# Optimization experiments

Hardware: AMD Instinct MI355X
Metric: run time of the kernel (lower is better)

## Reference

```python
import jax, jax.numpy as jnp
import numpy as np


def setup_inputs() -> dict:
    key = jax.random.key(0)
    k1, k2 = jax.random.split(key)
    B, S, H = 8, 4096, 1024
    sequence_output = jax.random.normal(k1, (B, S, H), dtype=jnp.float32)
    # labels in {0,1}: no -100 padding so the mask-compaction has a static shape
    sent_token_mask = jax.random.randint(k2, (B, S), 0, 2, dtype=jnp.int64)
    return {"sequence_output": sequence_output, "sent_token_mask": sent_token_mask}


def reference(sequence_output, sent_token_mask):
    B, S, H = sequence_output.shape
    # mask compaction: all positions valid (labels in {0,1}), so it's a reshape
    sent_features = sequence_output.reshape(B * S, H)  # [B*S, H]

    labels = sent_token_mask  # [B, S]
    # seg_id assigned BEFORE processing each label; increments AFTER label==0
    inc = (labels == 0).astype(jnp.int32).reshape(B * S)
    within = jnp.cumsum(inc) - inc  # exclusive prefix sum of increments
    # extra increment at end of each example whose last label == 1
    extra = (labels[:, -1] == 1).astype(jnp.int32)  # [B]
    extra_off = jnp.cumsum(extra) - extra           # exclusive over examples
    topic_segment_ids = within.reshape(B, S) + extra_off[:, None]
    return sent_features, topic_segment_ids.reshape(B * S)
```

## Files before the change

kernel.cpp:

```cpp
#include <hip/hip_runtime.h>

constexpr int Bn  = 8;
constexpr int Sn  = 4096;
constexpr int Nn  = Bn * Sn;
constexpr int Hn  = 1024;

constexpr int TPB = 256;
constexpr int NW  = TPB / 64;
constexpr int G4    = Nn / 4;
constexpr int ITERS = G4 / TPB;

constexpr size_t FEAT_ELEMS = (size_t)Nn * Hn;
constexpr size_t FEAT_VEC4  = FEAT_ELEMS / 4;
constexpr int    VEC_PER_T  = 8;
constexpr int    COPY_BLOCKS = (int)(FEAT_VEC4 / ((size_t)TPB * VEC_PER_T));

typedef float v4f __attribute__((ext_vector_type(4)));

__global__ __launch_bounds__(TPB) void fused_kernel(const float* __restrict__ seq,
                                                    const int* __restrict__ labels,
                                                    float* __restrict__ out) {
    if (blockIdx.x > 0) {
        const v4f* __restrict__ src = reinterpret_cast<const v4f*>(seq);
        v4f* __restrict__ dst       = reinterpret_cast<v4f*>(out);
        const size_t base = (size_t)(blockIdx.x - 1) * (TPB * VEC_PER_T) + threadIdx.x;
        v4f r[VEC_PER_T];
#pragma unroll
        for (int i = 0; i < VEC_PER_T; ++i)
            r[i] = __builtin_nontemporal_load(&src[base + (size_t)i * TPB]);
#pragma unroll
        for (int i = 0; i < VEC_PER_T; ++i)
            __builtin_nontemporal_store(r[i], &dst[base + (size_t)i * TPB]);
        return;
    }

    __shared__ int range_pre[TPB];
    __shared__ int wave_sums[NW];
    __shared__ int extra_off_sh[Bn];

    const int tid  = threadIdx.x;
    const int lane = tid & 63;
    const int hl   = lane & 31;
    const int wave = tid >> 6;

    const int4* __restrict__ lab4 = reinterpret_cast<const int4*>(labels);
    v4f* __restrict__ seg4 = reinterpret_cast<v4f*>(out + FEAT_ELEMS);

#pragma unroll 4
    for (int i = 0; i < ITERS; ++i) {
        const int g = i * TPB + tid;
        int4 v = lab4[g];
        int c = (v.x == 0) + (v.y == 0) + (v.z == 0) + (v.w == 0);
#pragma unroll
        for (int k = 1; k < 32; k <<= 1) c += __shfl_xor(c, k, 32);
        if (hl == 0) range_pre[g >> 5] = c;
    }

    if (tid == 0) {
        int acc = 0;
#pragma unroll
        for (int b = 0; b < Bn; ++b) {
            extra_off_sh[b] = acc;
            acc += (labels[b * Sn + Sn - 1] == 1);
        }
    }
    __syncthreads();

    const int s = range_pre[tid];
    int incl = s;
#pragma unroll
    for (int off = 1; off < 64; off <<= 1) {
        int u = __shfl_up(incl, off, 64);
        if (lane >= off) incl += u;
    }
    if (lane == 63) wave_sums[wave] = incl;
    __syncthreads();

    if (wave == 0) {
        int v = (lane < NW) ? wave_sums[lane] : 0;
#pragma unroll
        for (int off = 1; off < NW; off <<= 1) {
            int u = __shfl_up(v, off, 64);
            if (lane >= off) v += u;
        }
        if (lane < NW) wave_sums[lane] = v;
    }
    __syncthreads();

    range_pre[tid] = (wave ? wave_sums[wave - 1] : 0) + (incl - s);
    __syncthreads();

#pragma unroll 4
    for (int i = 0; i < ITERS; ++i) {
        const int g = i * TPB + tid;
        int4 v = lab4[g];
        const int f0 = (v.x == 0), f1 = (v.y == 0), f2 = (v.z == 0), f3 = (v.w == 0);
        const int c = f0 + f1 + f2 + f3;
        int pc = c;
#pragma unroll
        for (int off = 1; off < 32; off <<= 1) {
            int u = __shfl_up(pc, off, 32);
            if (hl >= off) pc += u;
        }
        const int base = range_pre[g >> 5] + extra_off_sh[g >> 10] + (pc - c);
        v4f r;
        r.x = (float)base;
        r.y = (float)(base + f0);
        r.z = (float)(base + f0 + f1);
        r.w = (float)(base + f0 + f1 + f2);
        __builtin_nontemporal_store(r, &seg4[g]);
    }
}

extern "C" void kernel_launch(void* const* d_in, const int* in_sizes, int n_in,
                              void* d_out, int out_size, void* d_ws, size_t ws_size,
                              hipStream_t stream) {
    const float* seq    = (const float*)d_in[0];
    const int*   labels = (const int*)d_in[1];
    float*       out    = (float*)d_out;

    fused_kernel<<<COPY_BLOCKS + 1, TPB, 0, stream>>>(seq, labels, out);
}
```

Baseline: 233.4 us.

## Split feature copy into hipMemcpyAsync and single-pass tiled segment scan

Replaces the fused kernel's copy blocks with a device-to-device hipMemcpyAsync for the 128 MiB feature tensor. The segment-id computation becomes its own one-block, 1024-thread kernel that does a single-pass tiled scan with a running carry and prefetching, instead of reading the labels twice. The aim is to use the runtime's optimized copy path and shorten the scan. In exchange the copy and the scan now run one after another rather than concurrently, and there are two launches instead of one.

After: 234.1 us. Within noise of the previous version (+0.3%).

```diff
diff --git a/kernel.cpp b/kernel.cpp
--- a/kernel.cpp
+++ b/kernel.cpp
@@ -5,110 +5,77 @@
 constexpr int Nn  = Bn * Sn;
 constexpr int Hn  = 1024;
 
-constexpr int TPB = 256;
-constexpr int NW  = TPB / 64;
+constexpr size_t FEAT_ELEMS = (size_t)Nn * Hn;
+constexpr size_t FEAT_BYTES = FEAT_ELEMS * sizeof(float);
+
+constexpr int STPB  = 1024;
+constexpr int SNW   = STPB / 64;
 constexpr int G4    = Nn / 4;
-constexpr int ITERS = G4 / TPB;
-
-constexpr size_t FEAT_ELEMS = (size_t)Nn * Hn;
-constexpr size_t FEAT_VEC4  = FEAT_ELEMS / 4;
-constexpr int    VEC_PER_T  = 8;
-constexpr int    COPY_BLOCKS = (int)(FEAT_VEC4 / ((size_t)TPB * VEC_PER_T));
+constexpr int TILES = G4 / STPB;
 
 typedef float v4f __attribute__((ext_vector_type(4)));
 
-__global__ __launch_bounds__(TPB) void fused_kernel(const float* __restrict__ seq,
-                                                    const int* __restrict__ labels,
-                                                    float* __restrict__ out) {
-    if (blockIdx.x > 0) {
-        const v4f* __restrict__ src = reinterpret_cast<const v4f*>(seq);
-        v4f* __restrict__ dst       = reinterpret_cast<v4f*>(out);
-        const size_t base = (size_t)(blockIdx.x - 1) * (TPB * VEC_PER_T) + threadIdx.x;
-        v4f r[VEC_PER_T];
-#pragma unroll
-        for (int i = 0; i < VEC_PER_T; ++i)
-            r[i] = __builtin_nontemporal_load(&src[base + (size_t)i * TPB]);
-#pragma unroll
-        for (int i = 0; i < VEC_PER_T; ++i)
-            __builtin_nontemporal_store(r[i], &dst[base + (size_t)i * TPB]);
-        return;
-    }
-
-    __shared__ int range_pre[TPB];
-    __shared__ int wave_sums[NW];
-    __shared__ int extra_off_sh[Bn];
+__global__ __launch_bounds__(STPB) void seg_kernel(const int* __restrict__ labels,
+                                                   float* __restrict__ out) {
+    __shared__ int wsums[SNW];
+    __shared__ int extra_sh[Bn];
 
     const int tid  = threadIdx.x;
     const int lane = tid & 63;
-    const int hl   = lane & 31;
     const int wave = tid >> 6;
 
     const int4* __restrict__ lab4 = reinterpret_cast<const int4*>(labels);
     v4f* __restrict__ seg4 = reinterpret_cast<v4f*>(out + FEAT_ELEMS);
 
-#pragma unroll 4
-    for (int i = 0; i < ITERS; ++i) {
-        const int g = i * TPB + tid;
-        int4 v = lab4[g];
-        int c = (v.x == 0) + (v.y == 0) + (v.z == 0) + (v.w == 0);
-#pragma unroll
-        for (int k = 1; k < 32; k <<= 1) c += __shfl_xor(c, k, 32);
-        if (hl == 0) range_pre[g >> 5] = c;
-    }
-
     if (tid == 0) {
         int acc = 0;
 #pragma unroll
         for (int b = 0; b < Bn; ++b) {
-            extra_off_sh[b] = acc;
+            extra_sh[b] = acc;
             acc += (labels[b * Sn + Sn - 1] == 1);
         }
     }
+
+    int carry = 0;
+    int4 v = lab4[tid];
     __syncthreads();
 
-    const int s = range_pre[tid];
-    int incl = s;
-#pragma unroll
-    for (int off = 1; off < 64; off <<= 1) {
-        int u = __shfl_up(incl, off, 64);
-        if (lane >= off) incl += u;
-    }
-    if (lane == 63) wave_sums[wave] = incl;
-    __syncthreads();
+    for (int k = 0; k < TILES; ++k) {
+        int4 nv;
+        if (k + 1 < TILES) nv = lab4[(k + 1) * STPB + tid];
 
-    if (wave == 0) {
-        int v = (lane < NW) ? wave_sums[lane] : 0;
-#pragma unroll
-        for (int off = 1; off < NW; off <<= 1) {
-            int u = __shfl_up(v, off, 64);
-            if (lane >= off) v += u;
-        }
-        if (lane < NW) wave_sums[lane] = v;
-    }
-    __syncthreads();
-
-    range_pre[tid] = (wave ? wave_sums[wave - 1] : 0) + (incl - s);
-    __syncthreads();
-
-#pragma unroll 4
-    for (int i = 0; i < ITERS; ++i) {
-        const int g = i * TPB + tid;
-        int4 v = lab4[g];
         const int f0 = (v.x == 0), f1 = (v.y == 0), f2 = (v.z == 0), f3 = (v.w == 0);
         const int c = f0 + f1 + f2 + f3;
-        int pc = c;
+
+        int incl = c;
 #pragma unroll
-        for (int off = 1; off < 32; off <<= 1) {
-            int u = __shfl_up(pc, off, 32);
-            if (hl >= off) pc += u;
+        for (int off = 1; off < 64; off <<= 1) {
+            int u = __shfl_up(incl, off, 64);
+            if (lane >= off) incl += u;
         }
-        const int base = range_pre[g >> 5] + extra_off_sh[g >> 10] + (pc - c);
+        if (lane == 63) wsums[wave] = incl;
+        __syncthreads();
+
+        int wexcl = 0, tot = 0;
+#pragma unroll
+        for (int w = 0; w < SNW; ++w) {
+            int s = wsums[w];
+            wexcl += (w < wave) ? s : 0;
+            tot   += s;
+        }
+
+        const int g    = k * STPB + tid;
+        const int base = carry + wexcl + (incl - c) + extra_sh[g >> 10];
         v4f r;
         r.x = (float)base;
         r.y = (float)(base + f0);
         r.z = (float)(base + f0 + f1);
         r.w = (float)(base + f0 + f1 + f2);
         __builtin_nontemporal_store(r, &seg4[g]);
+
+        carry += tot;
+        __syncthreads();
+        v = nv;
     }
 }
 
@@ -119,5 +86,7 @@
     const int*   labels = (const int*)d_in[1];
     float*       out    = (float*)d_out;
 
-    fused_kernel<<<COPY_BLOCKS + 1, TPB, 0, stream>>>(seq, labels, out);
+    seg_kernel<<<1, STPB, 0, stream>>>(labels, out);
+
+    hipMemcpyAsync(out, seq, FEAT_BYTES, hipMemcpyDeviceToDevice, stream);
 }
```
